# Performance work log

Measured on AMD Instinct MI355X. Metric: run time of the kernel, lower is better.

The kernel has to match this reference:

```python
import jax, jax.numpy as jnp
import numpy as np

NUM_RELS = 8

def _rgcn_layer(x, src, dst, rel, W, Wroot, b, num_rels):
    # PyG RGCNConv with aggr='mean': out = bias + x @ root + sum_r mean_{e in rel r, dst=i} (x[src_e] @ W_r)
    # mean-then-transform == transform-then-mean (linear), so transform first.
    N = x.shape[0]
    xW = jnp.einsum('nf,rfg->rng', x, W)            # [R, N, G] per-relation transformed features
    comb = dst * num_rels + rel                       # combined (node, relation) segment id
    deg = jax.ops.segment_sum(jnp.ones(rel.shape, x.dtype), comb, num_segments=N * num_rels)
    norm = 1.0 / jnp.maximum(deg[comb], 1.0)          # 1/deg_r(dst) per edge
    msg = xW[rel, src] * norm[:, None]                # [E, G]
    agg = jax.ops.segment_sum(msg, dst, num_segments=N)
    return agg + x @ Wroot + b


def setup_inputs() -> dict:
    key = jax.random.key(0)
    ks = jax.random.split(key, 10)
    N, E, R = 50000, 800000, NUM_RELS
    F_in, H, O = 256, 256, 128
    x = jax.random.normal(ks[0], (N, F_in), dtype=jnp.float32)
    edge_index = jax.random.randint(ks[1], (2, E), 0, N, dtype=jnp.int64)
    edge_type = jax.random.randint(ks[2], (E,), 0, R, dtype=jnp.int64)
    s1 = 1.0 / np.sqrt(F_in)
    s2 = 1.0 / np.sqrt(H)
    W1 = jax.random.normal(ks[3], (R, F_in, H), dtype=jnp.float32) * s1
    root1 = jax.random.normal(ks[4], (F_in, H), dtype=jnp.float32) * s1
    b1 = jnp.zeros((H,), dtype=jnp.float32)
    W2 = jax.random.normal(ks[5], (R, H, O), dtype=jnp.float32) * s2
    root2 = jax.random.normal(ks[6], (H, O), dtype=jnp.float32) * s2
    b2 = jnp.zeros((O,), dtype=jnp.float32)
    return {"x": x, "edge_index": edge_index, "edge_type": edge_type,
            "W1": W1, "root1": root1, "b1": b1,
            "W2": W2, "root2": root2, "b2": b2}


def reference(x, edge_index, edge_type, W1, root1, b1, W2, root2, b2):
    src, dst = edge_index[0], edge_index[1]
    h = jax.nn.relu(_rgcn_layer(x, src, dst, edge_type, W1, root1, b1, NUM_RELS))
    return _rgcn_layer(h, src, dst, edge_type, W2, root2, b2, NUM_RELS)
```

## Files before the change

### kernel.cpp

```cpp
#include <hip/hip_runtime.h>
#include <stdint.h>

#define RELS 8
#define F 256
#define KDIM 2304
#define NKT 36
#define TSZ 8192
#define SCAN_CHUNK 1024


typedef __attribute__((ext_vector_type(8))) short short8;
typedef __attribute__((ext_vector_type(4))) float f32x4;
typedef __attribute__((ext_vector_type(2))) unsigned int uint2v;

__device__ __forceinline__ unsigned short f2bf(float f) {
  union { float f; unsigned int u; } v; v.f = f;
  unsigned int u = v.u;
  if ((u & 0x7f800000u) == 0x7f800000u) return (unsigned short)(u >> 16);
  return (unsigned short)((u + 0x7fffu + ((u >> 16) & 1u)) >> 16);
}
__device__ __forceinline__ float bf2f(unsigned short b) {
  union { unsigned int u; float f; } v; v.u = ((unsigned int)b) << 16; return v.f;
}

#define GLOAD_LDS16(g, l)                                              \
  __builtin_amdgcn_global_load_lds(                                    \
      (const __attribute__((address_space(1))) void*)(g),              \
      (__attribute__((address_space(3))) void*)(l), 16, 0, 0)

__global__ void k_xb(const float* __restrict__ x, unsigned short* __restrict__ xb, int N) {
  int tid = blockIdx.x * blockDim.x + threadIdx.x;
  int n = tid >> 6, q = tid & 63;
  if (n >= N) return;
  const float4 v = *(const float4*)&x[(size_t)n * F + q * 4];
  ushort4 o;
  o.x = f2bf(v.x); o.y = f2bf(v.y); o.z = f2bf(v.z); o.w = f2bf(v.w);
  *(ushort4*)&xb[(size_t)n * F + q * 4] = o;
}

__global__ void k_wt(const float* __restrict__ W, const float* __restrict__ root,
                     unsigned short* __restrict__ Wt, int Ncols) {
  int tid = blockIdx.x * blockDim.x + threadIdx.x;
  int total = Ncols * KDIM;
  if (tid >= total) return;
  int n = tid / KDIM, k = tid - n * KDIM;
  float v = (k < 2048) ? W[(size_t)k * Ncols + n] : root[(size_t)(k - 2048) * Ncols + n];
  int tile = n >> 7, row = n & 127;
  int kt = k >> 6, c = k & 63;
  int u = ((c >> 3) + row) & 7;
  Wt[(size_t)(tile * NKT + kt) * TSZ + row * 64 + u * 8 + (c & 7)] = f2bf(v);
}

__global__ void k_count(const int* __restrict__ ei, const int* __restrict__ et,
                        int* __restrict__ cnt, int E) {
  int e = blockIdx.x * blockDim.x + threadIdx.x;
  if (e >= E) return;
  int bin = ei[E + e] * RELS + et[e];
  atomicAdd(&cnt[bin], 1);
}

__global__ void k_scan1(const int* __restrict__ cnt, int* __restrict__ start,
                        int* __restrict__ bsum, int nb) {
  __shared__ int tsum[256];
  const int t = threadIdx.x;
  const int idx = blockIdx.x * SCAN_CHUNK + t * 4;
  int v[4]; int s = 0;
#pragma unroll
  for (int i = 0; i < 4; i++) { v[i] = (idx + i < nb) ? cnt[idx + i] : 0; s += v[i]; }
  tsum[t] = s;
  __syncthreads();
  for (int d = 1; d < 256; d <<= 1) {
    int a = (t >= d) ? tsum[t - d] : 0;
    __syncthreads();
    tsum[t] += a;
    __syncthreads();
  }
  int ex = (t > 0) ? tsum[t - 1] : 0;
#pragma unroll
  for (int i = 0; i < 4; i++) { if (idx + i < nb) start[idx + i] = ex; ex += v[i]; }
  if (t == 255) bsum[blockIdx.x] = tsum[255];
}

__global__ void k_scan2(int* __restrict__ bsum, int nblocks) {
  __shared__ int sh[1024];
  const int t = threadIdx.x;
  sh[t] = (t < nblocks) ? bsum[t] : 0;
  __syncthreads();
  for (int d = 1; d < 1024; d <<= 1) {
    int a = (t >= d) ? sh[t - d] : 0;
    __syncthreads();
    sh[t] += a;
    __syncthreads();
  }
  if (t < nblocks) bsum[t] = (t > 0) ? sh[t - 1] : 0;
  if (t == 1023) bsum[nblocks] = sh[1023];
}

__global__ void k_scan3(int* __restrict__ start, const int* __restrict__ bsum,
                        int nb, int nblocks) {
  int i = blockIdx.x * blockDim.x + threadIdx.x;
  if (i < nb) start[i] += bsum[i >> 10];
  if (i == 0) start[nb] = bsum[nblocks];
}

__global__ void k_scatter(const int* __restrict__ ei, const int* __restrict__ et,
                          const int* __restrict__ start, int* __restrict__ cur,
                          int* __restrict__ ssrc, int E) {
  int e = blockIdx.x * blockDim.x + threadIdx.x;
  if (e >= E) return;
  int bin = ei[E + e] * RELS + et[e];
  int p = atomicAdd(&cur[bin], 1);
  ssrc[start[bin] + p] = ei[e];
}

__global__ void k_agg(const unsigned short* __restrict__ src,
                      const int* __restrict__ start, const int* __restrict__ ssrc,
                      unsigned short* __restrict__ A, int nbins) {
  int w = blockIdx.x * 4 + (threadIdx.x >> 6);
  int lane = threadIdx.x & 63;
  if (w >= nbins) return;
  int s0 = start[w], s1 = start[w + 1];
  int deg = s1 - s0;
  float scale = 1.0f / (float)(deg > 1 ? deg : 1);
  float a0 = 0.f, a1 = 0.f, a2 = 0.f, a3 = 0.f;
  int e = s0;
  for (; e + 1 < s1; e += 2) {
    int sA = ssrc[e], sB = ssrc[e + 1];
    const ushort4 vA = *(const ushort4*)&src[(size_t)sA * F + lane * 4];
    const ushort4 vB = *(const ushort4*)&src[(size_t)sB * F + lane * 4];
    a0 += bf2f(vA.x) + bf2f(vB.x); a1 += bf2f(vA.y) + bf2f(vB.y);
    a2 += bf2f(vA.z) + bf2f(vB.z); a3 += bf2f(vA.w) + bf2f(vB.w);
  }
  if (e < s1) {
    int sA = ssrc[e];
    const ushort4 vA = *(const ushort4*)&src[(size_t)sA * F + lane * 4];
    a0 += bf2f(vA.x); a1 += bf2f(vA.y); a2 += bf2f(vA.z); a3 += bf2f(vA.w);
  }
  int n = w >> 3, r = w & 7;
  int tile = n >> 7, row = n & 127;
  int kt = r * 4 + (lane >> 4);
  int u = (((lane & 15) >> 1) + row) & 7;
  uint2v o;
  o.x = (unsigned)f2bf(a0 * scale) | ((unsigned)f2bf(a1 * scale) << 16);
  o.y = (unsigned)f2bf(a2 * scale) | ((unsigned)f2bf(a3 * scale) << 16);
  __builtin_nontemporal_store(o,
      (uint2v*)&A[(size_t)(tile * NKT + kt) * TSZ + row * 64 + u * 8 + (lane & 1) * 4]);
}

__global__ void k_copy_nt(const unsigned short* __restrict__ src, unsigned short* __restrict__ A, int N) {
  int tid = blockIdx.x * blockDim.x + threadIdx.x;
  int n = tid >> 6, q = tid & 63;
  if (n >= N) return;
  const uint2v v = *(const uint2v*)&src[(size_t)n * F + q * 4];
  int tile = n >> 7, row = n & 127;
  int kt = 32 + (q >> 4);
  int u = (((q & 15) >> 1) + row) & 7;
  __builtin_nontemporal_store(v,
      (uint2v*)&A[(size_t)(tile * NKT + kt) * TSZ + row * 64 + u * 8 + (q & 1) * 4]);
}

template<bool RELU, bool OUTBF16>
__global__ __launch_bounds__(256) void k_gemm(
    const unsigned short* __restrict__ Ag, const unsigned short* __restrict__ Bg,
    const float* __restrict__ bias, void* __restrict__ outp,
    int Nld, int Mreal) {
  __shared__ unsigned short As[2][TSZ];
  __shared__ unsigned short Bs[2][TSZ];
  const int t = threadIdx.x;
  const int m0 = blockIdx.x * 128;
  const int n0 = blockIdx.y * 128;
  const int lane = t & 63, wid = t >> 6;
  const int wm = (wid >> 1) * 64, wn = (wid & 1) * 64;
  const int c15 = lane & 15, quad = lane >> 4;

  f32x4 acc[4][4];
#pragma unroll
  for (int i = 0; i < 4; i++)
#pragma unroll
    for (int j = 0; j < 4; j++) acc[i][j] = (f32x4)0.f;

  const unsigned short* Abase = Ag + (size_t)blockIdx.x * NKT * TSZ;
  const unsigned short* Bbase = Bg + (size_t)blockIdx.y * NKT * TSZ;

#define STAGE(buf, kt_)                                                      \
  {                                                                          \
    const unsigned short* ac = Abase + (size_t)(kt_) * TSZ;                  \
    const unsigned short* bc = Bbase + (size_t)(kt_) * TSZ;                  \
    _Pragma("unroll")                                                        \
    for (int j = 0; j < 4; j++) {                                            \
      GLOAD_LDS16(ac + j * 2048 + t * 8, &As[buf][j * 2048 + t * 8]);        \
      GLOAD_LDS16(bc + j * 2048 + t * 8, &Bs[buf][j * 2048 + t * 8]);        \
    }                                                                        \
  }

#define COMPUTE(buf)                                                         \
  {                                                                          \
    _Pragma("unroll")                                                        \
    for (int kk = 0; kk < 2; kk++) {                                         \
      short8 af[4], bf[4];                                                   \
      _Pragma("unroll")                                                      \
      for (int mi = 0; mi < 4; mi++) {                                       \
        int row = wm + mi * 16 + c15;                                        \
        int u = ((kk * 4 + quad) + row) & 7;                                 \
        af[mi] = *(const short8*)&As[buf][row * 64 + u * 8];                 \
      }                                                                      \
      _Pragma("unroll")                                                      \
      for (int ni = 0; ni < 4; ni++) {                                       \
        int row = wn + ni * 16 + c15;                                        \
        int u = ((kk * 4 + quad) + row) & 7;                                 \
        bf[ni] = *(const short8*)&Bs[buf][row * 64 + u * 8];                 \
      }                                                                      \
      __builtin_amdgcn_s_setprio(1);                                         \
      _Pragma("unroll")                                                      \
      for (int mi = 0; mi < 4; mi++)                                         \
        _Pragma("unroll")                                                    \
        for (int ni = 0; ni < 4; ni++)                                       \
          acc[mi][ni] = __builtin_amdgcn_mfma_f32_16x16x32_bf16(             \
              af[mi], bf[ni], acc[mi][ni], 0, 0, 0);                         \
      __builtin_amdgcn_s_setprio(0);                                         \
    }                                                                        \
  }

  STAGE(0, 0);
  __syncthreads();
#pragma unroll 1
  for (int kt = 0; kt < NKT; kt += 2) {
    STAGE(1, kt + 1);
    COMPUTE(0);
    __syncthreads();
    if (kt + 2 < NKT) STAGE(0, kt + 2);
    COMPUTE(1);
    __syncthreads();
  }
#undef STAGE
#undef COMPUTE

#pragma unroll
  for (int mi = 0; mi < 4; mi++) {
#pragma unroll
    for (int ni = 0; ni < 4; ni++) {
      int n = n0 + wn + ni * 16 + c15;
      float bv = bias[n];
#pragma unroll
      for (int r = 0; r < 4; r++) {
        int m = m0 + wm + mi * 16 + quad * 4 + r;
        if (m < Mreal) {
          float v = acc[mi][ni][r] + bv;
          if (RELU) v = v > 0.f ? v : 0.f;
          if (OUTBF16) ((unsigned short*)outp)[(size_t)m * Nld + n] = f2bf(v);
          else         ((float*)outp)[(size_t)m * Nld + n] = v;
        }
      }
    }
  }
}

extern "C" void kernel_launch(void* const* d_in, const int* in_sizes, int n_in,
                              void* d_out, int out_size, void* d_ws, size_t ws_size,
                              hipStream_t stream) {
  const float* x     = (const float*)d_in[0];
  const int*   ei    = (const int*)d_in[1];
  const int*   et    = (const int*)d_in[2];
  const float* W1    = (const float*)d_in[3];
  const float* root1 = (const float*)d_in[4];
  const float* b1    = (const float*)d_in[5];
  const float* W2    = (const float*)d_in[6];
  const float* root2 = (const float*)d_in[7];
  const float* b2    = (const float*)d_in[8];

  const int N = in_sizes[0] / F;
  const int E = in_sizes[2];
  const int nbins = N * RELS;
  const int Mpad = ((N + 127) / 128) * 128;
  const int ntiles = Mpad / 128;
  const int nsb = (nbins + SCAN_CHUNK - 1) / SCAN_CHUNK;

  char* base = (char*)d_ws;
  size_t off = 0;
  auto alloc = [&](size_t bytes) {
    void* r = base + off;
    off = (off + bytes + 511) & ~(size_t)511;
    return r;
  };
  unsigned short* Wt1  = (unsigned short*)alloc((size_t)2 * NKT * TSZ * 2);
  unsigned short* Wt2  = (unsigned short*)alloc((size_t)1 * NKT * TSZ * 2);
  int*            cnt  = (int*)alloc((size_t)nbins * 4);
  int*            strt = (int*)alloc((size_t)(nbins + 1) * 4);
  int*            bsum = (int*)alloc((size_t)(nsb + 1) * 4);
  int*            ssrc = (int*)alloc((size_t)E * 4);
  unsigned short* xh   = (unsigned short*)alloc((size_t)Mpad * F * 2);
  unsigned short* A    = (unsigned short*)alloc((size_t)ntiles * NKT * TSZ * 2);
  (void)ws_size; (void)n_in; (void)out_size;

  hipMemsetAsync(cnt, 0, (size_t)nbins * 4, stream);
  k_xb<<<(N * 64 + 255) / 256, 256, 0, stream>>>(x, xh, N);
  k_wt<<<(256 * KDIM + 255) / 256, 256, 0, stream>>>(W1, root1, Wt1, 256);
  k_wt<<<(128 * KDIM + 255) / 256, 256, 0, stream>>>(W2, root2, Wt2, 128);
  k_count<<<(E + 255) / 256, 256, 0, stream>>>(ei, et, cnt, E);
  k_scan1<<<nsb, 256, 0, stream>>>(cnt, strt, bsum, nbins);
  k_scan2<<<1, 1024, 0, stream>>>(bsum, nsb);
  k_scan3<<<(nbins + 255) / 256, 256, 0, stream>>>(strt, bsum, nbins, nsb);
  hipMemsetAsync(cnt, 0, (size_t)nbins * 4, stream);
  k_scatter<<<(E + 255) / 256, 256, 0, stream>>>(ei, et, strt, cnt, ssrc, E);

  k_agg<<<(nbins + 3) / 4, 256, 0, stream>>>(xh, strt, ssrc, A, nbins);
  k_copy_nt<<<(N * 64 + 255) / 256, 256, 0, stream>>>(xh, A, N);
  k_gemm<true, true><<<dim3(ntiles, 2), 256, 0, stream>>>(A, Wt1, b1, xh, 256, N);

  k_agg<<<(nbins + 3) / 4, 256, 0, stream>>>(xh, strt, ssrc, A, nbins);
  k_copy_nt<<<(N * 64 + 255) / 256, 256, 0, stream>>>(xh, A, N);
  k_gemm<false, false><<<dim3(ntiles, 1), 256, 0, stream>>>(A, Wt2, b2, d_out, 128, N);
}
```

Before: 620.5 us.

## Load GEMM fragments directly from global into registers, skipping LDS staging

```diff
diff --git a/kernel.cpp b/kernel.cpp
--- a/kernel.cpp
+++ b/kernel.cpp
@@ -22,11 +22,6 @@
 __device__ __forceinline__ float bf2f(unsigned short b) {
   union { unsigned int u; float f; } v; v.u = ((unsigned int)b) << 16; return v.f;
 }
-
-#define GLOAD_LDS16(g, l)                                              \
-  __builtin_amdgcn_global_load_lds(                                    \
-      (const __attribute__((address_space(1))) void*)(g),              \
-      (__attribute__((address_space(3))) void*)(l), 16, 0, 0)
 
 __global__ void k_xb(const float* __restrict__ x, unsigned short* __restrict__ xb, int N) {
   int tid = blockIdx.x * blockDim.x + threadIdx.x;
@@ -160,79 +155,78 @@
 }
 
 template<bool RELU, bool OUTBF16>
-__global__ __launch_bounds__(256) void k_gemm(
+__global__ __launch_bounds__(256, 2) void k_gemm(
     const unsigned short* __restrict__ Ag, const unsigned short* __restrict__ Bg,
     const float* __restrict__ bias, void* __restrict__ outp,
     int Nld, int Mreal) {
-  __shared__ unsigned short As[2][TSZ];
-  __shared__ unsigned short Bs[2][TSZ];
   const int t = threadIdx.x;
-  const int m0 = blockIdx.x * 128;
-  const int n0 = blockIdx.y * 128;
+  const int m0 = blockIdx.y * 128;
+  const int n0 = blockIdx.x * 128;
   const int lane = t & 63, wid = t >> 6;
   const int wm = (wid >> 1) * 64, wn = (wid & 1) * 64;
   const int c15 = lane & 15, quad = lane >> 4;
 
+  int offA[4][2], offB[4][2];
+#pragma unroll
+  for (int i = 0; i < 4; i++) {
+#pragma unroll
+    for (int kk = 0; kk < 2; kk++) {
+      int rowA = wm + i * 16 + c15;
+      offA[i][kk] = rowA * 64 + ((((kk * 4 + quad) + rowA) & 7) * 8);
+      int rowB = wn + i * 16 + c15;
+      offB[i][kk] = rowB * 64 + ((((kk * 4 + quad) + rowB) & 7) * 8);
+    }
+  }
+
   f32x4 acc[4][4];
 #pragma unroll
   for (int i = 0; i < 4; i++)
 #pragma unroll
     for (int j = 0; j < 4; j++) acc[i][j] = (f32x4)0.f;
 
-  const unsigned short* Abase = Ag + (size_t)blockIdx.x * NKT * TSZ;
-  const unsigned short* Bbase = Bg + (size_t)blockIdx.y * NKT * TSZ;
-
-#define STAGE(buf, kt_)                                                      \
+  const unsigned short* Abase = Ag + (size_t)blockIdx.y * NKT * TSZ;
+  const unsigned short* Bbase = Bg + (size_t)blockIdx.x * NKT * TSZ;
+
+  short8 a0[4][2], b0[4][2], a1[4][2], b1[4][2];
+
+#define LOADF(A_, B_, kt_)                                                   \
   {                                                                          \
-    const unsigned short* ac = Abase + (size_t)(kt_) * TSZ;                  \
-    const unsigned short* bc = Bbase + (size_t)(kt_) * TSZ;                  \
+    const unsigned short* ap = Abase + (size_t)(kt_) * TSZ;                  \
+    const unsigned short* bp = Bbase + (size_t)(kt_) * TSZ;                  \
     _Pragma("unroll")                                                        \
-    for (int j = 0; j < 4; j++) {                                            \
-      GLOAD_LDS16(ac + j * 2048 + t * 8, &As[buf][j * 2048 + t * 8]);        \
-      GLOAD_LDS16(bc + j * 2048 + t * 8, &Bs[buf][j * 2048 + t * 8]);        \
+    for (int i = 0; i < 4; i++) {                                            \
+      _Pragma("unroll")                                                      \
+      for (int kk = 0; kk < 2; kk++) {                                       \
+        A_[i][kk] = *(const short8*)(ap + offA[i][kk]);                      \
+        B_[i][kk] = *(const short8*)(bp + offB[i][kk]);                      \
+      }                                                                      \
     }                                                                        \
   }
 
-#define COMPUTE(buf)                                                         \
+#define COMPUTE(A_, B_)                                                      \
   {                                                                          \
     _Pragma("unroll")                                                        \
-    for (int kk = 0; kk < 2; kk++) {                                         \
-      short8 af[4], bf[4];                                                   \
-      _Pragma("unroll")                                                      \
-      for (int mi = 0; mi < 4; mi++) {                                       \
-        int row = wm + mi * 16 + c15;                                        \
-        int u = ((kk * 4 + quad) + row) & 7;                                 \
-        af[mi] = *(const short8*)&As[buf][row * 64 + u * 8];                 \
-      }                                                                      \
-      _Pragma("unroll")                                                      \
-      for (int ni = 0; ni < 4; ni++) {                                       \
-        int row = wn + ni * 16 + c15;                                        \
-        int u = ((kk * 4 + quad) + row) & 7;                                 \
-        bf[ni] = *(const short8*)&Bs[buf][row * 64 + u * 8];                 \
-      }                                                                      \
-      __builtin_amdgcn_s_setprio(1);                                         \
+    for (int kk = 0; kk < 2; kk++)                                           \
       _Pragma("unroll")                                                      \
       for (int mi = 0; mi < 4; mi++)                                         \
         _Pragma("unroll")                                                    \
         for (int ni = 0; ni < 4; ni++)                                       \
           acc[mi][ni] = __builtin_amdgcn_mfma_f32_16x16x32_bf16(             \
-              af[mi], bf[ni], acc[mi][ni], 0, 0, 0);                         \
-      __builtin_amdgcn_s_setprio(0);                                         \
-    }                                                                        \
-  }
-
-  STAGE(0, 0);
-  __syncthreads();
+              A_[mi][kk], B_[ni][kk], acc[mi][ni], 0, 0, 0);                 \
+  }
+
+  LOADF(a0, b0, 0);
+  LOADF(a1, b1, 1);
 #pragma unroll 1
-  for (int kt = 0; kt < NKT; kt += 2) {
-    STAGE(1, kt + 1);
-    COMPUTE(0);
-    __syncthreads();
-    if (kt + 2 < NKT) STAGE(0, kt + 2);
-    COMPUTE(1);
-    __syncthreads();
-  }
-#undef STAGE
+  for (int kt = 0; kt < NKT - 2; kt += 2) {
+    COMPUTE(a0, b0);
+    LOADF(a0, b0, kt + 2);
+    COMPUTE(a1, b1);
+    LOADF(a1, b1, kt + 3);
+  }
+  COMPUTE(a0, b0);
+  COMPUTE(a1, b1);
+#undef LOADF
 #undef COMPUTE
 
 #pragma unroll
@@ -305,9 +299,9 @@
 
   k_agg<<<(nbins + 3) / 4, 256, 0, stream>>>(xh, strt, ssrc, A, nbins);
   k_copy_nt<<<(N * 64 + 255) / 256, 256, 0, stream>>>(xh, A, N);
-  k_gemm<true, true><<<dim3(ntiles, 2), 256, 0, stream>>>(A, Wt1, b1, xh, 256, N);
+  k_gemm<true, true><<<dim3(2, ntiles), 256, 0, stream>>>(A, Wt1, b1, xh, 256, N);
 
   k_agg<<<(nbins + 3) / 4, 256, 0, stream>>>(xh, strt, ssrc, A, nbins);
   k_copy_nt<<<(N * 64 + 255) / 256, 256, 0, stream>>>(xh, A, N);
-  k_gemm<false, false><<<dim3(ntiles, 1), 256, 0, stream>>>(A, Wt2, b2, d_out, 128, N);
-}
+  k_gemm<false, false><<<dim3(1, ntiles), 256, 0, stream>>>(A, Wt2, b2, d_out, 128, N);
+}
```

Result: slower. 761.0 us (+22.6%).
